# Kernel tuning notes

Hardware: AMD Instinct MI355X
Metric: run time of the kernel (lower is better)

The kernel has to match this reference:

```python
import jax, jax.numpy as jnp
import numpy as np

HIDDEN = 4096
NUM_HEADS = 32
HEAD_DIM = 128
NUM_KV_HEADS = 8
KV_GROUPS = NUM_HEADS // NUM_KV_HEADS
ROPE_THETA = 10000.0
SEQ = 2048
BATCH = 1
NEG_INF = -1e9


def fake_quant_int8(x):
    """Per-tensor symmetric int8 fake quantization (absmax scale)."""
    scale = jnp.maximum(jnp.max(jnp.abs(x)) / 127.0, 1e-8)
    q = jnp.clip(jnp.round(x / scale), -127.0, 127.0) * scale
    # straight-through estimator (no-op in fwd-only, keeps code shared)
    return x + jax.lax.stop_gradient(q - x)


def rotate_half(x):
    x1, x2 = jnp.split(x, 2, axis=-1)
    return jnp.concatenate([-x2, x1], axis=-1)


def rope_cos_sin(position_ids):
    inv_freq = 1.0 / (ROPE_THETA ** (jnp.arange(0, HEAD_DIM, 2, dtype=jnp.float32) / HEAD_DIM))
    freqs = position_ids.astype(jnp.float32)[..., None] * inv_freq  # [B,S,HD/2]
    emb = jnp.concatenate([freqs, freqs], axis=-1)                  # [B,S,HD]
    return jnp.cos(emb), jnp.sin(emb)


def setup_inputs() -> dict:
    key = jax.random.key(0)
    k1, k2, k3, k4, k5 = jax.random.split(key, 5)
    hidden_states = jax.random.normal(k1, (BATCH, SEQ, HIDDEN), dtype=jnp.float32)
    causal = jnp.tril(jnp.ones((SEQ, SEQ), dtype=bool))
    attention_mask = jnp.where(causal, 0.0, NEG_INF).astype(jnp.float32)[None, None]  # [1,1,S,S]
    position_ids = jnp.arange(SEQ, dtype=jnp.int64 if jax.config.jax_enable_x64 else jnp.int32)[None, :]
    s = 0.02
    wq = jax.random.normal(k2, (NUM_HEADS * HEAD_DIM, HIDDEN), dtype=jnp.float32) * s
    wk = jax.random.normal(k3, (NUM_KV_HEADS * HEAD_DIM, HIDDEN), dtype=jnp.float32) * s
    wv = jax.random.normal(k4, (NUM_KV_HEADS * HEAD_DIM, HIDDEN), dtype=jnp.float32) * s
    wo = jax.random.normal(k5, (HIDDEN, NUM_HEADS * HEAD_DIM), dtype=jnp.float32) * s
    return {"hidden_states": hidden_states, "attention_mask": attention_mask,
            "position_ids": position_ids, "wq": wq, "wk": wk, "wv": wv, "wo": wo}


def reference(hidden_states, attention_mask, position_ids, wq, wk, wv, wo):
    B, S, _ = hidden_states.shape

    def qlinear(x, w):  # quantized linear: fake-quant act and weight, y = x @ w.T
        return fake_quant_int8(x) @ fake_quant_int8(w).T

    q = qlinear(hidden_states, wq).reshape(B, S, NUM_HEADS, HEAD_DIM).transpose(0, 2, 1, 3)
    k = qlinear(hidden_states, wk).reshape(B, S, NUM_KV_HEADS, HEAD_DIM).transpose(0, 2, 1, 3)
    v = qlinear(hidden_states, wv).reshape(B, S, NUM_KV_HEADS, HEAD_DIM).transpose(0, 2, 1, 3)

    cos, sin = rope_cos_sin(position_ids)      # [B,S,HD]
    cos, sin = cos[:, None], sin[:, None]      # [B,1,S,HD]
    q = q * cos + rotate_half(q) * sin
    k = k * cos + rotate_half(k) * sin

    # repeat_kv: GQA -> full heads
    k = jnp.repeat(k, KV_GROUPS, axis=1)
    v = jnp.repeat(v, KV_GROUPS, axis=1)

    # quantized QK^T
    scores = jnp.einsum('bhqd,bhkd->bhqk', fake_quant_int8(q), fake_quant_int8(k))
    scores = scores * (1.0 / np.sqrt(HEAD_DIM).astype(np.float32))
    scores = scores + attention_mask[:, :, :, :S]
    probs = jax.nn.softmax(scores.astype(jnp.float32), axis=-1).astype(q.dtype)
    # attention_dropout = 0.0 -> identity

    # quantized AV
    attn_out = jnp.einsum('bhqk,bhkd->bhqd', fake_quant_int8(probs), fake_quant_int8(v))
    attn_out = attn_out.transpose(0, 2, 1, 3).reshape(B, S, NUM_HEADS * HEAD_DIM)
    return qlinear(attn_out, wo)
```

## Files before the change

### kernel.cpp

```cpp
#include <hip/hip_runtime.h>
#include <hip/hip_fp16.h>
#include <stdint.h>

#define SEQ   2048
#define HID   4096
#define NH    32
#define NKV   8
#define KVDIM 1024
#define KVCAT 2048

typedef int v4i __attribute__((ext_vector_type(4)));

#define VMCNT0 asm volatile("s_waitcnt vmcnt(0)" ::: "memory")

__device__ __forceinline__ void gload16(const void* g, void* l) {
    __builtin_amdgcn_global_load_lds(
        (const __attribute__((address_space(1))) void*)(uintptr_t)g,
        (__attribute__((address_space(3))) void*)(uintptr_t)l, 16, 0, 0);
}

__device__ __forceinline__ float slot_scale(const unsigned* slots, int slot) {
    return fmaxf(__uint_as_float(slots[slot << 5]) / 127.0f, 1e-8f);
}

__device__ __forceinline__ int q8v(float x, float s) {
    int v = (int)rintf(x / s);
    return v < -127 ? -127 : (v > 127 ? 127 : v);
}

__device__ __forceinline__ unsigned pk4(float a, float b, float c, float d, float s) {
    return (unsigned)(uint8_t)(int8_t)q8v(a, s)
         | ((unsigned)(uint8_t)(int8_t)q8v(b, s) << 8)
         | ((unsigned)(uint8_t)(int8_t)q8v(c, s) << 16)
         | ((unsigned)(uint8_t)(int8_t)q8v(d, s) << 24);
}

__device__ __forceinline__ float fexp2(float x) {
    float r; asm("v_exp_f32 %0, %1" : "=v"(r) : "v"(x)); return r;
}

__device__ __forceinline__ float fmax4a(float4 x) {
    return fmaxf(fmaxf(fabsf(x.x), fabsf(x.y)), fmaxf(fabsf(x.z), fabsf(x.w)));
}

__device__ __forceinline__ void block_amax_part(float m, float* dst) {
    __shared__ float sm[4];
    int lane = threadIdx.x & 63, w = threadIdx.x >> 6;
    for (int off = 32; off; off >>= 1) m = fmaxf(m, __shfl_xor(m, off, 64));
    if (lane == 0) sm[w] = m;
    __syncthreads();
    if (threadIdx.x == 0)
        *dst = fmaxf(fmaxf(sm[0], sm[1]), fmaxf(sm[2], sm[3]));
    __syncthreads();
}

#define NV0 ((long)SEQ * HID / 4)
#define NV1 ((long)HID * HID / 4)
#define NV2 ((long)KVDIM * HID / 4)
__global__ void k_absmax5(const float* __restrict__ a0, const float* __restrict__ a1,
                          const float* __restrict__ a2, const float* __restrict__ a3,
                          const float* __restrict__ a4, float* __restrict__ part) {
    int b = blockIdx.x;
    const float* p; long n; int lb, nb;
    if (b < 342)       { p = a0; n = NV0; lb = b;        nb = 342; }
    else if (b < 1025) { p = a1; n = NV1; lb = b - 342;  nb = 683; }
    else if (b < 1196) { p = a2; n = NV2; lb = b - 1025; nb = 171; }
    else if (b < 1367) { p = a3; n = NV2; lb = b - 1196; nb = 171; }
    else               { p = a4; n = NV1; lb = b - 1367; nb = 681; }
    long str = (long)nb * 256;
    float mm[8] = {0.f, 0.f, 0.f, 0.f, 0.f, 0.f, 0.f, 0.f};
    long v = (long)lb * 256 + threadIdx.x;
    for (; v + 7 * str < n; v += 8 * str) {
        float4 t[8];
        #pragma unroll
        for (int j = 0; j < 8; j++) t[j] = *(const float4*)(p + (v + j * str) * 4);
        #pragma unroll
        for (int j = 0; j < 8; j++) mm[j] = fmaxf(mm[j], fmax4a(t[j]));
    }
    for (; v < n; v += str) mm[0] = fmaxf(mm[0], fmax4a(*(const float4*)(p + v * 4)));
    float m = fmaxf(fmaxf(fmaxf(mm[0], mm[1]), fmaxf(mm[2], mm[3])),
                    fmaxf(fmaxf(mm[4], mm[5]), fmaxf(mm[6], mm[7])));
    block_amax_part(m, part + blockIdx.x);
}

__global__ void k_reduceA(const float* __restrict__ part, unsigned* slots) {
    __shared__ float sm[4];
    const int lo[5] = {0, 342, 1025, 1196, 1367};
    const int hi[5] = {342, 1025, 1196, 1367, 2048};
    int t = threadIdx.x, lane = t & 63, w = t >> 6;
    for (int s = 0; s < 5; s++) {
        float m = 0.f;
        for (int i = lo[s] + t; i < hi[s]; i += 256) m = fmaxf(m, part[i]);
        for (int off = 32; off; off >>= 1) m = fmaxf(m, __shfl_xor(m, off, 64));
        if (lane == 0) sm[w] = m;
        __syncthreads();
        if (t == 0)
            slots[s << 5] = __float_as_uint(fmaxf(fmaxf(sm[0], sm[1]), fmaxf(sm[2], sm[3])));
        __syncthreads();
    }
}

__global__ void k_reduceB(const float* __restrict__ p1, const float* __restrict__ p2,
                          const float* __restrict__ p3, unsigned* slots) {
    __shared__ float sm[4];
    int t = threadIdx.x, lane = t & 63, w = t >> 6;
    const float* ps[3] = {p1, p2, p3};
    const int cnt[3] = {512, 128, 128};
    const int sl[3] = {5, 6, 7};
    for (int s = 0; s < 3; s++) {
        float m = 0.f;
        for (int i = t; i < cnt[s]; i += 256) m = fmaxf(m, ps[s][i]);
        for (int off = 32; off; off >>= 1) m = fmaxf(m, __shfl_xor(m, off, 64));
        if (lane == 0) sm[w] = m;
        __syncthreads();
        if (t == 0)
            slots[sl[s] << 5] = __float_as_uint(fmaxf(fmaxf(sm[0], sm[1]), fmaxf(sm[2], sm[3])));
        __syncthreads();
    }
}

#define NU0 ((long)SEQ * HID / 16)
#define NU1 ((long)HID * HID / 16)
#define NU2 ((long)KVDIM * HID / 16)
__global__ void k_quant4(const float* __restrict__ a0, const float* __restrict__ a1,
                         const float* __restrict__ a2, const float* __restrict__ a3,
                         int8_t* __restrict__ d0, int8_t* __restrict__ d1,
                         int8_t* __restrict__ d2, int8_t* __restrict__ d3,
                         const unsigned* __restrict__ slots) {
    int b = blockIdx.x;
    const float* p; int8_t* d; long n; int slot, lb, nb;
    if (b < 512)       { p = a0; d = d0; n = NU0; slot = 0; lb = b;        nb = 512; }
    else if (b < 1536) { p = a1; d = d1; n = NU1; slot = 1; lb = b - 512;  nb = 1024; }
    else if (b < 1792) { p = a2; d = d2; n = NU2; slot = 2; lb = b - 1536; nb = 256; }
    else               { p = a3; d = d3; n = NU2; slot = 3; lb = b - 1792; nb = 256; }
    float s = slot_scale(slots, slot);
    long str = (long)nb * 256;
    for (long u = (long)lb * 256 + threadIdx.x; u < n; u += str) {
        const float4* src = (const float4*)(p + u * 16);
        float4 t0 = src[0], t1 = src[1], t2 = src[2], t3 = src[3];
        int4 o;
        o.x = (int)pk4(t0.x, t0.y, t0.z, t0.w, s);
        o.y = (int)pk4(t1.x, t1.y, t1.z, t1.w, s);
        o.z = (int)pk4(t2.x, t2.y, t2.z, t2.w, s);
        o.w = (int)pk4(t3.x, t3.y, t3.z, t3.w, s);
        *(int4*)(d + u * 16) = o;
    }
}

__global__ void k_quantw(const float* __restrict__ x, int8_t* __restrict__ q, long nu,
                         const unsigned* __restrict__ slots, int slot) {
    float s = slot_scale(slots, slot);
    long gs = (long)gridDim.x * blockDim.x;
    for (long u = blockIdx.x * (long)blockDim.x + threadIdx.x; u < nu; u += gs) {
        const float4* src = (const float4*)(x + u * 16);
        float4 t0 = src[0], t1 = src[1], t2 = src[2], t3 = src[3];
        int4 o;
        o.x = (int)pk4(t0.x, t0.y, t0.z, t0.w, s);
        o.y = (int)pk4(t1.x, t1.y, t1.z, t1.w, s);
        o.z = (int)pk4(t2.x, t2.y, t2.z, t2.w, s);
        o.w = (int)pk4(t3.x, t3.y, t3.z, t3.w, s);
        *(int4*)(q + u * 16) = o;
    }
}

__device__ __forceinline__ unsigned pk4h(unsigned h2a, unsigned h2b, float s) {
    __half2 a = *(__half2*)&h2a, b = *(__half2*)&h2b;
    return pk4(__low2float(a), __high2float(a), __low2float(b), __high2float(b), s);
}
__global__ void k_quanth(const __half* __restrict__ x, int8_t* __restrict__ q, long nu,
                         int rshift, long cmask, long ld,
                         const unsigned* __restrict__ slots, int slot) {
    float s = slot_scale(slots, slot);
    long gs = (long)gridDim.x * blockDim.x;
    for (long u = blockIdx.x * (long)blockDim.x + threadIdx.x; u < nu; u += gs) {
        long row = u >> rshift;
        long cu = u & cmask;
        const int4* src = (const int4*)(x + row * ld + cu * 16);
        int4 a = src[0], b = src[1];
        int4 o;
        o.x = (int)pk4h((unsigned)a.x, (unsigned)a.y, s);
        o.y = (int)pk4h((unsigned)a.z, (unsigned)a.w, s);
        o.z = (int)pk4h((unsigned)b.x, (unsigned)b.y, s);
        o.w = (int)pk4h((unsigned)b.z, (unsigned)b.w, s);
        *(int4*)(q + u * 16) = o;
    }
}

__global__ void k_ropetab(const int* __restrict__ pos, float* __restrict__ ct,
                          float* __restrict__ st) {
    int tid = blockIdx.x * blockDim.x + threadIdx.x;
    if (tid >= SEQ * 64) return;
    int i = tid & 63, s = tid >> 6;
    double inv = 1.0 / pow(10000.0, (double)((float)(2 * i) * (1.0f / 128.0f)));
    float invf = (float)inv;
    float angf = (float)pos[s] * invf;
    double a = (double)angf;
    ct[tid] = (float)cos(a);
    st[tid] = (float)sin(a);
}

__global__ void k_transq(const __half* __restrict__ src, long lds_, int8_t* __restrict__ dst,
                         long ldd, const unsigned* __restrict__ slots, int slot) {
    __shared__ float t[32][33];
    float s = slot_scale(slots, slot);
    int bx = blockIdx.x, by = blockIdx.y;
    int tid = threadIdx.x;
    int c = tid & 31, r0 = tid >> 5;
    #pragma unroll
    for (int j = 0; j < 4; j++) {
        int r = r0 + j * 8;
        t[r][c] = __half2float(src[(long)(by * 32 + r) * lds_ + bx * 32 + c]);
    }
    __syncthreads();
    int d = tid >> 3, k4 = (tid & 7) * 4;
    unsigned pa = 0;
    #pragma unroll
    for (int j = 0; j < 4; j++) {
        int iv = q8v(t[k4 + j][d], s);
        pa |= ((unsigned)(uint8_t)(int8_t)iv) << (8 * j);
    }
    *(unsigned*)(dst + (long)(bx * 32 + d) * ldd + by * 32 + k4) = pa;
}

__global__ __launch_bounds__(256) void k_gemm_i8(
    const int8_t* __restrict__ A, const int8_t* __restrict__ B, void* __restrict__ Cv,
    int M, int N, int K, unsigned* slots,
    int slotA, int slotB, int slotB2, int nsplit,
    float* pQ, float* pK, float* pV, int ropemode,
    const float* __restrict__ ct, const float* __restrict__ st) {
    __shared__ int8_t POOL[65536];
    int8_t (*As)[16384] = (int8_t(*)[16384])POOL;
    int8_t (*Bs)[16384] = (int8_t(*)[16384])(POOL + 32768);
    float* Cf = (float*)Cv;
    __half* Ch = (__half*)Cv;
    const v4i vzero = {0, 0, 0, 0};
    int tid = threadIdx.x, lane = tid & 63, wid = tid >> 6;
    int nbx = N >> 7;
    int nwg = gridDim.x, wg = blockIdx.x;
    int cpx = nwg >> 3;
    int swz = (wg & 7) * cpx + (wg >> 3);
    int bm = swz / nbx, bn = swz % nbx;
    long rowA0 = (long)bm * 128, colB0 = (long)bn * 128;
    int wrow = (wid >> 1) * 64, wcol = (wid & 1) * 64;
    int lr = lane >> 3;
    int swc = ((lane & 7) ^ lr) * 16;
    const int8_t* ga = A + (rowA0 + wid * 8 + lr) * (long)K + swc;
    const int8_t* gb = B + (colB0 + wid * 8 + lr) * (long)K + swc;
    v4i acc[4][4];
    #pragma unroll
    for (int m = 0; m < 4; m++)
        #pragma unroll
        for (int n = 0; n < 4; n++) acc[m][n] = vzero;

    auto STAGE = [&](int buf, int kt) {
        #pragma unroll
        for (int i = 0; i < 4; i++) {
            gload16(ga + kt + (long)(i * 32) * K, &As[buf][(wid * 8 + i * 32) * 128]);
            gload16(gb + kt + (long)(i * 32) * K, &Bs[buf][(wid * 8 + i * 32) * 128]);
        }
    };
    auto COMPUTE = [&](int buf) {
        #pragma unroll
        for (int ks = 0; ks < 2; ks++) {
            v4i af[4], bf[4];
            #pragma unroll
            for (int m = 0; m < 4; m++) {
                int row = wrow + m * 16 + (lane & 15);
                af[m] = *(const v4i*)(&As[buf][row * 128 + (((ks * 4 + (lane >> 4)) ^ (row & 7)) * 16)]);
            }
            #pragma unroll
            for (int n = 0; n < 4; n++) {
                int row = wcol + n * 16 + (lane & 15);
                bf[n] = *(const v4i*)(&Bs[buf][row * 128 + (((ks * 4 + (lane >> 4)) ^ (row & 7)) * 16)]);
            }
            #pragma unroll
            for (int m = 0; m < 4; m++)
                #pragma unroll
                for (int n = 0; n < 4; n++)
                    acc[m][n] = __builtin_amdgcn_mfma_i32_16x16x64_i8(af[m], bf[n], acc[m][n], 0, 0, 0);
        }
    };

    STAGE(0, 0);
    VMCNT0;
    __syncthreads();
    int nt = K >> 7, cur = 0;
    for (int t = 0; t < nt - 1; t++) {
        STAGE(cur ^ 1, (t + 1) << 7);
        COMPUTE(cur);
        VMCNT0;
        __syncthreads();
        cur ^= 1;
    }
    COMPUTE(cur);

    float sA = slot_scale(slots, slotA);
    float sB1 = slot_scale(slots, slotB);
    float sB2 = slot_scale(slots, slotB2);
    int qc = lane & 15, rgrp = (lane >> 4) << 2;
    if (ropemode == 1 || (ropemode == 2 && bn < 8)) {
        __syncthreads();
        float* EX = (float*)POOL;
        #pragma unroll
        for (int m = 0; m < 4; m++)
            #pragma unroll
            for (int n = 0; n < 4; n++) {
                int coll = wcol + n * 16 + qc;
                #pragma unroll
                for (int r = 0; r < 4; r++) {
                    int rowl = wrow + m * 16 + rgrp + r;
                    EX[rowl * 128 + (coll ^ ((rowl & 1) << 4))] = sA * sB1 * (float)acc[m][n][r];
                }
            }
        __syncthreads();
        float am = 0.f;
        #pragma unroll
        for (int m = 0; m < 4; m++)
            #pragma unroll
            for (int n = 0; n < 4; n++) {
                int coll = wcol + n * 16 + qc;
                #pragma unroll
                for (int r = 0; r < 4; r++) {
                    int rowl = wrow + m * 16 + rgrp + r;
                    long srow = rowA0 + rowl;
                    float self = EX[rowl * 128 + (coll ^ ((rowl & 1) << 4))];
                    float pv = EX[rowl * 128 + ((coll ^ 64) ^ ((rowl & 1) << 4))];
                    float c = ct[srow * 64 + (coll & 63)];
                    float sn = st[srow * 64 + (coll & 63)];
                    float o = (coll < 64) ? self * c - pv * sn : self * c + pv * sn;
                    am = fmaxf(am, fabsf(o));
                    Ch[srow * N + colB0 + coll] = __float2half(o);
                }
            }
        block_amax_part(am, (ropemode == 1) ? pQ + blockIdx.x : pK + bm * 8 + (bn & 7));
    } else if (ropemode == 2) {
        float am = 0.f;
        #pragma unroll
        for (int m = 0; m < 4; m++) {
            long row0 = rowA0 + wrow + m * 16 + rgrp;
            #pragma unroll
            for (int n = 0; n < 4; n++) {
                int col = (int)colB0 + wcol + n * 16 + qc;
                float sc = sA * ((col < nsplit) ? sB1 : sB2);
                __half* cp = Ch + row0 * N + col;
                #pragma unroll
                for (int r = 0; r < 4; r++) {
                    float val = sc * (float)acc[m][n][r];
                    cp[(long)r * N] = __float2half(val);
                    am = fmaxf(am, fabsf(val));
                }
            }
        }
        block_amax_part(am, pV + bm * 8 + (bn & 7));
    } else {
        #pragma unroll
        for (int m = 0; m < 4; m++) {
            long row0 = rowA0 + wrow + m * 16 + rgrp;
            #pragma unroll
            for (int n = 0; n < 4; n++) {
                int col = (int)colB0 + wcol + n * 16 + qc;
                float sc = sA * ((col < nsplit) ? sB1 : sB2);
                float* cp = Cf + row0 * N + col;
                #pragma unroll
                for (int r = 0; r < 4; r++) cp[(long)r * N] = sc * (float)acc[m][n][r];
            }
        }
    }
}

__global__ __launch_bounds__(256) void k_attn(
    const int8_t* __restrict__ Qq, const int8_t* __restrict__ Kq, const int8_t* __restrict__ Vtq,
    __half* __restrict__ AO, unsigned* slots) {
    __shared__ int8_t Qs[64 * 128];
    __shared__ int8_t Ks[2][64 * 128];
    __shared__ int8_t Vs[2][128 * 64];
    __shared__ int smx[4];
    const v4i vzero = {0, 0, 0, 0};
    const int NEGS = -(1 << 29);
    const float MAGIC = 12582912.0f;
    int tid = threadIdx.x, lane = tid & 63, w = tid >> 6;
    int qlan = lane & 15, g = lane >> 4;
    int idx = blockIdx.x;
    int qb = 31 - (idx >> 5), h = idx & 31, kvh = h >> 2;
    float sq = slot_scale(slots, 5), sk = slot_scale(slots, 6);
    float spv = slot_scale(slots, 7) * (1.0f / 127.0f);
    float c2 = sq * sk * 0.08838834764831845f * 1.4426950408889634f;
    int lr8 = lane >> 3;
    int swc = ((lane & 7) ^ lr8) * 16;
    int lr4 = lane >> 2;
    int vswc = ((lane & 3) ^ (lr4 & 3)) * 16;
    const int8_t* kbase = Kq + ((long)(w * 8 + lr8)) * KVDIM + kvh * 128 + swc;
    const int8_t* vbase = Vtq + ((long)kvh * 128 + w * 16 + lr4) * SEQ + vswc;
    auto STAGE_K = [&](int buf, int kt) {
        #pragma unroll
        for (int i = 0; i < 2; i++)
            gload16(kbase + ((long)kt * 64 + i * 32) * KVDIM, &Ks[buf][(w * 8 + i * 32) * 128]);
    };
    auto STAGE_V = [&](int buf, int kt) {
        #pragma unroll
        for (int i = 0; i < 2; i++)
            gload16(vbase + (long)(i * 64) * SEQ + kt * 64, &Vs[buf][(w * 16 + i * 64) * 64]);
    };
    {
        const int8_t* qbase = Qq + ((long)qb * 64 + w * 8 + lr8) * HID + h * 128 + swc;
        #pragma unroll
        for (int i = 0; i < 2; i++)
            gload16(qbase + (long)(i * 32) * HID, &Qs[(w * 8 + i * 32) * 128]);
    }
    STAGE_K(0, 0);
    VMCNT0;
    __syncthreads();
    v4i aq[2];
    #pragma unroll
    for (int ks = 0; ks < 2; ks++) {
        int row = w * 16 + qlan;
        aq[ks] = *(const v4i*)(&Qs[row * 128 + (((ks * 4 + g) ^ (row & 7)) * 16)]);
    }
    int mi = -(1 << 30);
    float l = 0.f;
    int buf = 0;
    for (int kt = 0; kt <= qb; kt++) {
        if (kt < qb) STAGE_K(buf ^ 1, kt + 1);
        v4i sf[4] = {vzero, vzero, vzero, vzero};
        __builtin_amdgcn_s_setprio(1);
        #pragma unroll
        for (int ks = 0; ks < 2; ks++)
            #pragma unroll
            for (int f = 0; f < 4; f++) {
                int row = f * 16 + qlan;
                v4i bk = *(const v4i*)(&Ks[buf][row * 128 + (((ks * 4 + g) ^ (row & 7)) * 16)]);
                sf[f] = __builtin_amdgcn_mfma_i32_16x16x64_i8(bk, aq[ks], sf[f], 0, 0, 0);
            }
        __builtin_amdgcn_s_setprio(0);
        int sv[16];
        if (kt == qb) {
            int qthr = w * 16 + qlan;
            #pragma unroll
            for (int f = 0; f < 4; f++)
                #pragma unroll
                for (int r = 0; r < 4; r++) {
                    int kl = f * 16 + g * 4 + r;
                    sv[f * 4 + r] = (kl > qthr) ? NEGS : sf[f][r];
                }
        } else {
            #pragma unroll
            for (int f = 0; f < 4; f++)
                #pragma unroll
                for (int r = 0; r < 4; r++) sv[f * 4 + r] = sf[f][r];
        }
        int tm = sv[0];
        #pragma unroll
        for (int e = 1; e < 16; e++) tm = tm > sv[e] ? tm : sv[e];
        tm = max(tm, __shfl_xor(tm, 16, 64));
        tm = max(tm, __shfl_xor(tm, 32, 64));
        int mn = tm > mi ? tm : mi;
        float nb = -c2 * (float)mn;
        float esc = fexp2(fmaf((float)mi, c2, nb));
        float es = 0.f;
        #pragma unroll
        for (int e = 0; e < 16; e++) es += fexp2(fmaf((float)sv[e], c2, nb));
        es += __shfl_xor(es, 16, 64);
        es += __shfl_xor(es, 32, 64);
        l = l * esc + es;
        mi = mn;
        VMCNT0;
        __syncthreads();
        buf ^= 1;
    }
    float Bq = fmaf(c2, (float)mi, __log2f(l) - 6.9886846867721655f);
    unsigned* Ps32 = (unsigned*)Qs;
    int pwr = w * 320;
    v4i of[8];
    #pragma unroll
    for (int nf = 0; nf < 8; nf++) of[nf] = vzero;
    STAGE_K(0, 0);
    STAGE_V(0, 0);
    VMCNT0;
    __syncthreads();
    buf = 0;
    for (int kt = 0; kt <= qb; kt++) {
        if (kt < qb) { STAGE_K(buf ^ 1, kt + 1); STAGE_V(buf ^ 1, kt + 1); }
        v4i sf[4] = {vzero, vzero, vzero, vzero};
        __builtin_amdgcn_s_setprio(1);
        #pragma unroll
        for (int ks = 0; ks < 2; ks++)
            #pragma unroll
            for (int f = 0; f < 4; f++) {
                int row = f * 16 + qlan;
                v4i bk = *(const v4i*)(&Ks[buf][row * 128 + (((ks * 4 + g) ^ (row & 7)) * 16)]);
                sf[f] = __builtin_amdgcn_mfma_i32_16x16x64_i8(bk, aq[ks], sf[f], 0, 0, 0);
            }
        __builtin_amdgcn_s_setprio(0);
        if (kt == qb) {
            int qthr = w * 16 + qlan;
            #pragma unroll
            for (int f = 0; f < 4; f++) {
                unsigned pk = 0;
                #pragma unroll
                for (int r = 0; r < 4; r++) {
                    int kl = f * 16 + g * 4 + r;
                    int s = (kl > qthr) ? NEGS : sf[f][r];
                    float t = fexp2(fmaf((float)s, c2, -Bq));
                    unsigned u = __float_as_uint(t + MAGIC) & 127u;
                    pk |= u << (8 * r);
                }
                Ps32[pwr + (4 * f + g) * 20 + qlan] = pk;
            }
        } else {
            #pragma unroll
            for (int f = 0; f < 4; f++) {
                unsigned pk = 0;
                #pragma unroll
                for (int r = 0; r < 4; r++) {
                    float t = fexp2(fmaf((float)sf[f][r], c2, -Bq));
                    unsigned u = __float_as_uint(t + MAGIC) & 127u;
                    pk |= u << (8 * r);
                }
                Ps32[pwr + (4 * f + g) * 20 + qlan] = pk;
            }
        }
        int rb = pwr + 80 * g + qlan;
        v4i ap;
        ap[0] = (int)Ps32[rb];
        ap[1] = (int)Ps32[rb + 20];
        ap[2] = (int)Ps32[rb + 40];
        ap[3] = (int)Ps32[rb + 60];
        __builtin_amdgcn_s_setprio(1);
        #pragma unroll
        for (int nf = 0; nf < 8; nf++) {
            int row = nf * 16 + qlan;
            v4i bv = *(const v4i*)(&Vs[buf][row * 64 + ((g ^ (row & 3)) * 16)]);
            of[nf] = __builtin_amdgcn_mfma_i32_16x16x64_i8(ap, bv, of[nf], 0, 0, 0);
        }
        __builtin_amdgcn_s_setprio(0);
        VMCNT0;
        __syncthreads();
        buf ^= 1;
    }
    int mymax = 0;
    #pragma unroll
    for (int nf = 0; nf < 8; nf++)
        #pragma unroll
        for (int r = 0; r < 4; r++) {
            int val = of[nf][r];
            int av = val < 0 ? -val : val;
            mymax = av > mymax ? av : mymax;
            int qg = qb * 64 + w * 16 + 4 * g + r;
            AO[(long)qg * HID + h * 128 + nf * 16 + qlan] = __float2half(spv * (float)val);
        }
    #pragma unroll
    for (int off = 1; off < 64; off <<= 1) {
        int o2 = __shfl_xor(mymax, off, 64);
        mymax = o2 > mymax ? o2 : mymax;
    }
    if (lane == 0) smx[w] = mymax;
    __syncthreads();
    if (tid == 0) {
        int mm = max(max(smx[0], smx[1]), max(smx[2], smx[3]));
        atomicMax(slots + (8 << 5), (unsigned)mm);
    }
}

__global__ void k_quant_ao(const __half* __restrict__ a, int8_t* __restrict__ q,
                           unsigned* slots) {
    float sv = slot_scale(slots, 7);
    float spv = (1.0f / 127.0f) * sv;
    float amax = spv * (float)(int)slots[8 << 5];
    float s = fmaxf(amax / 127.0f, 1e-8f);
    long nu = (long)SEQ * HID / 16;
    long gs = (long)gridDim.x * blockDim.x;
    for (long u = blockIdx.x * (long)blockDim.x + threadIdx.x; u < nu; u += gs) {
        const int4* src = (const int4*)(a + u * 16);
        int4 x = src[0], y = src[1];
        int4 o;
        o.x = (int)pk4h((unsigned)x.x, (unsigned)x.y, s);
        o.y = (int)pk4h((unsigned)x.z, (unsigned)x.w, s);
        o.z = (int)pk4h((unsigned)y.x, (unsigned)y.y, s);
        o.w = (int)pk4h((unsigned)y.z, (unsigned)y.w, s);
        *(int4*)(q + u * 16) = o;
    }
    if (blockIdx.x == 0 && threadIdx.x == 0) slots[9 << 5] = __float_as_uint(amax);
}

extern "C" void kernel_launch(void* const* d_in, const int* in_sizes, int n_in,
                              void* d_out, int out_size, void* d_ws, size_t ws_size,
                              hipStream_t stream) {
    (void)in_sizes; (void)n_in; (void)out_size;
    const float* hid = (const float*)d_in[0];
    const int* pos = (const int*)d_in[2];
    const float* wqp = (const float*)d_in[3];
    const float* wkp = (const float*)d_in[4];
    const float* wvp = (const float*)d_in[5];
    const float* wop = (const float*)d_in[6];
    float* out = (float*)d_out;
    char* ws = (char*)d_ws;

    size_t o = 0;
    auto alloc = [&](size_t sz) { size_t r = o; o += (sz + 255) & ~(size_t)255; return r; };
    unsigned* slots = (unsigned*)(ws + alloc(2048));
    float* P0 = (float*)(ws + alloc(2048 * 4));
    float* P1 = (float*)(ws + alloc(512 * 4));
    float* P2 = (float*)(ws + alloc(128 * 4));
    float* P3 = (float*)(ws + alloc(128 * 4));
    int8_t* Xq   = (int8_t*)(ws + alloc((size_t)SEQ * HID));
    int8_t* Wqq  = (int8_t*)(ws + alloc((size_t)HID * HID));
    int8_t* Wkvq = (int8_t*)(ws + alloc((size_t)KVCAT * HID));
    __half* Qf   = (__half*)(ws + alloc((size_t)SEQ * HID * 2));
    __half* KVf  = (__half*)(ws + alloc((size_t)SEQ * KVCAT * 2));
    int8_t* Qq   = (int8_t*)(ws + alloc((size_t)SEQ * HID));
    int8_t* Kq   = (int8_t*)(ws + alloc((size_t)SEQ * KVDIM));
    int8_t* Vtq  = (int8_t*)(ws + alloc((size_t)KVDIM * SEQ));
    float*  ctab = (float*)(ws + alloc((size_t)SEQ * 64 * 4));
    float*  stab = (float*)(ws + alloc((size_t)SEQ * 64 * 4));
    if (ws_size < o) return;
    int8_t* Woq = Wqq;
    __half* AOh = Qf;
    int8_t* AOq = Xq;

    hipMemsetAsync(slots, 0, 2048, stream);
    k_ropetab<<<SEQ * 64 / 256, 256, 0, stream>>>(pos, ctab, stab);
    k_absmax5<<<2048, 256, 0, stream>>>(hid, wqp, wkp, wvp, wop, P0);
    k_reduceA<<<1, 256, 0, stream>>>(P0, slots);
    k_quant4<<<2048, 256, 0, stream>>>(hid, wqp, wkp, wvp,
                                       Xq, Wqq, Wkvq, Wkvq + (size_t)KVDIM * HID, slots);
    k_gemm_i8<<<512, 256, 0, stream>>>(Xq, Wqq, Qf, SEQ, HID, HID, slots,
                                       0, 1, 1, 1 << 30, P1, nullptr, nullptr, 1, ctab, stab);
    k_gemm_i8<<<256, 256, 0, stream>>>(Xq, Wkvq, KVf, SEQ, KVCAT, HID, slots,
                                       0, 2, 3, KVDIM, nullptr, P2, P3, 2, ctab, stab);
    k_quantw<<<1024, 256, 0, stream>>>(wop, Woq, (long)HID * HID / 16, slots, 4);
    k_reduceB<<<1, 256, 0, stream>>>(P1, P2, P3, slots);
    const long CALL = 0x3FFFFFFFL;
    k_quanth<<<1024, 256, 0, stream>>>(Qf, Qq, (long)SEQ * HID / 16, 40, CALL, 0, slots, 5);
    k_quanth<<<512, 256, 0, stream>>>(KVf, Kq, (long)SEQ * KVDIM / 16, 6, 63, KVCAT, slots, 6);
    k_transq<<<dim3(32, 64), 256, 0, stream>>>(KVf + KVDIM, KVCAT, Vtq, SEQ, slots, 7);
    k_attn<<<1024, 256, 0, stream>>>(Qq, Kq, Vtq, AOh, slots);
    k_quant_ao<<<1024, 256, 0, stream>>>(AOh, AOq, slots);
    k_gemm_i8<<<512, 256, 0, stream>>>(AOq, Woq, out, SEQ, HID, HID, slots,
                                       9, 4, 4, 1 << 30, nullptr, nullptr, nullptr, 0,
                                       nullptr, nullptr);
}
```

Before: 285.8 us.

## Skip negligible attention key tiles and fold Wo quantization into batched quant kernel

Result: slower. 291.8 us (+2.1%).

```diff
diff --git a/kernel.cpp b/kernel.cpp
--- a/kernel.cpp
+++ b/kernel.cpp
@@ -122,17 +122,20 @@
 #define NU0 ((long)SEQ * HID / 16)
 #define NU1 ((long)HID * HID / 16)
 #define NU2 ((long)KVDIM * HID / 16)
-__global__ void k_quant4(const float* __restrict__ a0, const float* __restrict__ a1,
+__global__ void k_quant5(const float* __restrict__ a0, const float* __restrict__ a1,
                          const float* __restrict__ a2, const float* __restrict__ a3,
+                         const float* __restrict__ a4,
                          int8_t* __restrict__ d0, int8_t* __restrict__ d1,
                          int8_t* __restrict__ d2, int8_t* __restrict__ d3,
+                         int8_t* __restrict__ d4,
                          const unsigned* __restrict__ slots) {
     int b = blockIdx.x;
     const float* p; int8_t* d; long n; int slot, lb, nb;
     if (b < 512)       { p = a0; d = d0; n = NU0; slot = 0; lb = b;        nb = 512; }
     else if (b < 1536) { p = a1; d = d1; n = NU1; slot = 1; lb = b - 512;  nb = 1024; }
     else if (b < 1792) { p = a2; d = d2; n = NU2; slot = 2; lb = b - 1536; nb = 256; }
-    else               { p = a3; d = d3; n = NU2; slot = 3; lb = b - 1792; nb = 256; }
+    else if (b < 2048) { p = a3; d = d3; n = NU2; slot = 3; lb = b - 1792; nb = 256; }
+    else               { p = a4; d = d4; n = NU1; slot = 4; lb = b - 2048; nb = 512; }
     float s = slot_scale(slots, slot);
     long str = (long)nb * 256;
     for (long u = (long)lb * 256 + threadIdx.x; u < n; u += str) {
@@ -144,22 +147,6 @@
         o.z = (int)pk4(t2.x, t2.y, t2.z, t2.w, s);
         o.w = (int)pk4(t3.x, t3.y, t3.z, t3.w, s);
         *(int4*)(d + u * 16) = o;
-    }
-}
-
-__global__ void k_quantw(const float* __restrict__ x, int8_t* __restrict__ q, long nu,
-                         const unsigned* __restrict__ slots, int slot) {
-    float s = slot_scale(slots, slot);
-    long gs = (long)gridDim.x * blockDim.x;
-    for (long u = blockIdx.x * (long)blockDim.x + threadIdx.x; u < nu; u += gs) {
-        const float4* src = (const float4*)(x + u * 16);
-        float4 t0 = src[0], t1 = src[1], t2 = src[2], t3 = src[3];
-        int4 o;
-        o.x = (int)pk4(t0.x, t0.y, t0.z, t0.w, s);
-        o.y = (int)pk4(t1.x, t1.y, t1.z, t1.w, s);
-        o.z = (int)pk4(t2.x, t2.y, t2.z, t2.w, s);
-        o.w = (int)pk4(t3.x, t3.y, t3.z, t3.w, s);
-        *(int4*)(q + u * 16) = o;
     }
 }
 
@@ -224,7 +211,7 @@
 
 __global__ __launch_bounds__(256) void k_gemm_i8(
     const int8_t* __restrict__ A, const int8_t* __restrict__ B, void* __restrict__ Cv,
-    int M, int N, int K, unsigned* slots,
+    int N, int K, unsigned* slots,
     int slotA, int slotB, int slotB2, int nsplit,
     float* pQ, float* pK, float* pV, int ropemode,
     const float* __restrict__ ct, const float* __restrict__ st) {
@@ -375,6 +362,7 @@
     __shared__ int8_t Ks[2][64 * 128];
     __shared__ int8_t Vs[2][128 * 64];
     __shared__ int smx[4];
+    __shared__ int tmx[4][32][16];
     const v4i vzero = {0, 0, 0, 0};
     const int NEGS = -(1 << 29);
     const float MAGIC = 12582912.0f;
@@ -453,6 +441,7 @@
         for (int e = 1; e < 16; e++) tm = tm > sv[e] ? tm : sv[e];
         tm = max(tm, __shfl_xor(tm, 16, 64));
         tm = max(tm, __shfl_xor(tm, 32, 64));
+        tmx[w][kt][qlan] = tm;
         int mn = tm > mi ? tm : mi;
         float nb = -c2 * (float)mn;
         float esc = fexp2(fmaf((float)mi, c2, nb));
@@ -480,59 +469,63 @@
     buf = 0;
     for (int kt = 0; kt <= qb; kt++) {
         if (kt < qb) { STAGE_K(buf ^ 1, kt + 1); STAGE_V(buf ^ 1, kt + 1); }
-        v4i sf[4] = {vzero, vzero, vzero, vzero};
-        __builtin_amdgcn_s_setprio(1);
-        #pragma unroll
-        for (int ks = 0; ks < 2; ks++)
-            #pragma unroll
-            for (int f = 0; f < 4; f++) {
-                int row = f * 16 + qlan;
-                v4i bk = *(const v4i*)(&Ks[buf][row * 128 + (((ks * 4 + g) ^ (row & 7)) * 16)]);
-                sf[f] = __builtin_amdgcn_mfma_i32_16x16x64_i8(bk, aq[ks], sf[f], 0, 0, 0);
-            }
-        __builtin_amdgcn_s_setprio(0);
-        if (kt == qb) {
-            int qthr = w * 16 + qlan;
-            #pragma unroll
-            for (int f = 0; f < 4; f++) {
-                unsigned pk = 0;
-                #pragma unroll
-                for (int r = 0; r < 4; r++) {
-                    int kl = f * 16 + g * 4 + r;
-                    int s = (kl > qthr) ? NEGS : sf[f][r];
-                    float t = fexp2(fmaf((float)s, c2, -Bq));
-                    unsigned u = __float_as_uint(t + MAGIC) & 127u;
-                    pk |= u << (8 * r);
+        int tmv = tmx[w][kt][qlan];
+        int act = (fmaf(c2, (float)tmv, -Bq) > -1.0f);
+        if (__any(act)) {
+            v4i sf[4] = {vzero, vzero, vzero, vzero};
+            __builtin_amdgcn_s_setprio(1);
+            #pragma unroll
+            for (int ks = 0; ks < 2; ks++)
+                #pragma unroll
+                for (int f = 0; f < 4; f++) {
+                    int row = f * 16 + qlan;
+                    v4i bk = *(const v4i*)(&Ks[buf][row * 128 + (((ks * 4 + g) ^ (row & 7)) * 16)]);
+                    sf[f] = __builtin_amdgcn_mfma_i32_16x16x64_i8(bk, aq[ks], sf[f], 0, 0, 0);
                 }
-                Ps32[pwr + (4 * f + g) * 20 + qlan] = pk;
-            }
-        } else {
-            #pragma unroll
-            for (int f = 0; f < 4; f++) {
-                unsigned pk = 0;
-                #pragma unroll
-                for (int r = 0; r < 4; r++) {
-                    float t = fexp2(fmaf((float)sf[f][r], c2, -Bq));
-                    unsigned u = __float_as_uint(t + MAGIC) & 127u;
-                    pk |= u << (8 * r);
+            __builtin_amdgcn_s_setprio(0);
+            if (kt == qb) {
+                int qthr = w * 16 + qlan;
+                #pragma unroll
+                for (int f = 0; f < 4; f++) {
+                    unsigned pk = 0;
+                    #pragma unroll
+                    for (int r = 0; r < 4; r++) {
+                        int kl = f * 16 + g * 4 + r;
+                        int s = (kl > qthr) ? NEGS : sf[f][r];
+                        float t = fexp2(fmaf((float)s, c2, -Bq));
+                        unsigned u = __float_as_uint(t + MAGIC) & 127u;
+                        pk |= u << (8 * r);
+                    }
+                    Ps32[pwr + (4 * f + g) * 20 + qlan] = pk;
                 }
-                Ps32[pwr + (4 * f + g) * 20 + qlan] = pk;
-            }
+            } else {
+                #pragma unroll
+                for (int f = 0; f < 4; f++) {
+                    unsigned pk = 0;
+                    #pragma unroll
+                    for (int r = 0; r < 4; r++) {
+                        float t = fexp2(fmaf((float)sf[f][r], c2, -Bq));
+                        unsigned u = __float_as_uint(t + MAGIC) & 127u;
+                        pk |= u << (8 * r);
+                    }
+                    Ps32[pwr + (4 * f + g) * 20 + qlan] = pk;
+                }
+            }
+            int rb = pwr + 80 * g + qlan;
+            v4i ap;
+            ap[0] = (int)Ps32[rb];
+            ap[1] = (int)Ps32[rb + 20];
+            ap[2] = (int)Ps32[rb + 40];
+            ap[3] = (int)Ps32[rb + 60];
+            __builtin_amdgcn_s_setprio(1);
+            #pragma unroll
+            for (int nf = 0; nf < 8; nf++) {
+                int row = nf * 16 + qlan;
+                v4i bv = *(const v4i*)(&Vs[buf][row * 64 + ((g ^ (row & 3)) * 16)]);
+                of[nf] = __builtin_amdgcn_mfma_i32_16x16x64_i8(ap, bv, of[nf], 0, 0, 0);
+            }
+            __builtin_amdgcn_s_setprio(0);
         }
-        int rb = pwr + 80 * g + qlan;
-        v4i ap;
-        ap[0] = (int)Ps32[rb];
-        ap[1] = (int)Ps32[rb + 20];
-        ap[2] = (int)Ps32[rb + 40];
-        ap[3] = (int)Ps32[rb + 60];
-        __builtin_amdgcn_s_setprio(1);
-        #pragma unroll
-        for (int nf = 0; nf < 8; nf++) {
-            int row = nf * 16 + qlan;
-            v4i bv = *(const v4i*)(&Vs[buf][row * 64 + ((g ^ (row & 3)) * 16)]);
-            of[nf] = __builtin_amdgcn_mfma_i32_16x16x64_i8(ap, bv, of[nf], 0, 0, 0);
-        }
-        __builtin_amdgcn_s_setprio(0);
         VMCNT0;
         __syncthreads();
         buf ^= 1;
@@ -604,6 +597,7 @@
     float* P3 = (float*)(ws + alloc(128 * 4));
     int8_t* Xq   = (int8_t*)(ws + alloc((size_t)SEQ * HID));
     int8_t* Wqq  = (int8_t*)(ws + alloc((size_t)HID * HID));
+    int8_t* Woq  = (int8_t*)(ws + alloc((size_t)HID * HID));
     int8_t* Wkvq = (int8_t*)(ws + alloc((size_t)KVCAT * HID));
     __half* Qf   = (__half*)(ws + alloc((size_t)SEQ * HID * 2));
     __half* KVf  = (__half*)(ws + alloc((size_t)SEQ * KVCAT * 2));
@@ -613,7 +607,6 @@
     float*  ctab = (float*)(ws + alloc((size_t)SEQ * 64 * 4));
     float*  stab = (float*)(ws + alloc((size_t)SEQ * 64 * 4));
     if (ws_size < o) return;
-    int8_t* Woq = Wqq;
     __half* AOh = Qf;
     int8_t* AOq = Xq;
 
@@ -621,13 +614,12 @@
     k_ropetab<<<SEQ * 64 / 256, 256, 0, stream>>>(pos, ctab, stab);
     k_absmax5<<<2048, 256, 0, stream>>>(hid, wqp, wkp, wvp, wop, P0);
     k_reduceA<<<1, 256, 0, stream>>>(P0, slots);
-    k_quant4<<<2048, 256, 0, stream>>>(hid, wqp, wkp, wvp,
-                                       Xq, Wqq, Wkvq, Wkvq + (size_t)KVDIM * HID, slots);
-    k_gemm_i8<<<512, 256, 0, stream>>>(Xq, Wqq, Qf, SEQ, HID, HID, slots,
+    k_quant5<<<2560, 256, 0, stream>>>(hid, wqp, wkp, wvp, wop,
+                                       Xq, Wqq, Wkvq, Wkvq + (size_t)KVDIM * HID, Woq, slots);
+    k_gemm_i8<<<512, 256, 0, stream>>>(Xq, Wqq, Qf, HID, HID, slots,
                                        0, 1, 1, 1 << 30, P1, nullptr, nullptr, 1, ctab, stab);
-    k_gemm_i8<<<256, 256, 0, stream>>>(Xq, Wkvq, KVf, SEQ, KVCAT, HID, slots,
+    k_gemm_i8<<<256, 256, 0, stream>>>(Xq, Wkvq, KVf, KVCAT, HID, slots,
                                        0, 2, 3, KVDIM, nullptr, P2, P3, 2, ctab, stab);
-    k_quantw<<<1024, 256, 0, stream>>>(wop, Woq, (long)HID * HID / 16, slots, 4);
     k_reduceB<<<1, 256, 0, stream>>>(P1, P2, P3, slots);
     const long CALL = 0x3FFFFFFFL;
     k_quanth<<<1024, 256, 0, stream>>>(Qf, Qq, (long)SEQ * HID / 16, 40, CALL, 0, slots, 5);
@@ -635,7 +627,7 @@
     k_transq<<<dim3(32, 64), 256, 0, stream>>>(KVf + KVDIM, KVCAT, Vtq, SEQ, slots, 7);
     k_attn<<<1024, 256, 0, stream>>>(Qq, Kq, Vtq, AOh, slots);
     k_quant_ao<<<1024, 256, 0, stream>>>(AOh, AOq, slots);
-    k_gemm_i8<<<512, 256, 0, stream>>>(AOq, Woq, out, SEQ, HID, HID, slots,
+    k_gemm_i8<<<512, 256, 0, stream>>>(AOq, Woq, out, HID, HID, slots,
                                        9, 4, 4, 1 << 30, nullptr, nullptr, nullptr, 0,
                                        nullptr, nullptr);
 }
```
